# Optimization experiments

Hardware: AMD Instinct MI355X
Metric: run time of the kernel (lower is better)

The kernel has to match this reference:

```python
import jax, jax.numpy as jnp
import numpy as np

# ---- static config (mirrors AdaPKC2D_Thre init) ----
B, IN_CH, OUT_CH = 2, 16, 32
H, W = 256, 256
RB = 1                      # refer_band (must be 1 so ring has N=16 points)
GBH = [1, 2, 3, 4]
GBW = [1, 2, 3, 4]
THRESHOLD = 0.001
INIT_GB = (1, 1)
KH, KW = 4, 4
N = KH * KW                 # 16 sample points per pixel
PAD_H = GBH[-1] + RB        # padding[2]
PAD_W = GBW[-1] + RB        # padding[0]
W_PAD = W + 2 * PAD_W


def _uni_prf_grid(rb, gb):
    """16 (dx,dy) offsets on the guard-band ring (torch _get_uni_prf_grid)."""
    h_prf = (rb + gb[0]) * 2 + 1
    w_prf = (rb + gb[1]) * 2 + 1
    px, py = np.meshgrid(np.arange(-(rb + gb[0]), rb + gb[0] + 1),
                         np.arange(-(rb + gb[1]), rb + gb[1] + 1), indexing='ij')
    idx_td = np.round(np.linspace(0, (rb + gb[1]) * 2, 5)).astype(np.int64)
    idx_lr = np.round(np.linspace(0, (rb + gb[0]) * 2, 5)).astype(np.int64)[1:-1]

    def ring(a):
        return np.concatenate([a[0:rb, idx_td].ravel(),
                               a[idx_lr, w_prf - rb:w_prf].ravel(),
                               a[h_prf - rb:h_prf, idx_td].ravel(),
                               a[idx_lr, 0:rb].ravel()])
    return ring(px), ring(py)


def _build_offsets():
    offs, init_index = [], 0
    for gh in GBH:
        for gw in GBW:
            if gh == INIT_GB[0] and gw == INIT_GB[1]:
                init_index = len(offs)
            dx, dy = _uni_prf_grid(RB, (gh, gw))
            offs.append(dx * W_PAD + dy)  # flattened (row-major) offset
    return np.stack(offs, 0).astype(np.int32), init_index  # (G, N)

OFF_FLAT, INIT_INDEX = _build_offsets()
# flat index of each center pixel in the padded image, (H, W)
CIDX = ((np.arange(H) + PAD_H)[:, None] * W_PAD + (np.arange(W) + PAD_W)[None, :]).astype(np.int32)


def setup_inputs() -> dict:
    key = jax.random.key(0)
    k1, k2, k3 = jax.random.split(key, 3)
    x = jax.random.normal(k1, (B, IN_CH, H, W), dtype=jnp.float32)
    weight = jax.random.normal(k2, (OUT_CH, IN_CH, KH, KW), dtype=jnp.float32) * 0.05
    bias = jax.random.normal(k3, (OUT_CH,), dtype=jnp.float32) * 0.01
    return {"x": x, "weight": weight, "bias": bias}


def reference(x, weight, bias):
    b = x.shape[0]
    x_pad = jnp.pad(x, ((0, 0), (0, 0), (PAD_H, PAD_H), (PAD_W, PAD_W)))
    x_flat = x_pad.reshape(b, IN_CH, -1)                    # (b, c, Hp*Wp)
    cidx = jnp.asarray(CIDX)                                # (H, W)
    off = jnp.asarray(OFF_FLAT)                             # (G, N)

    # center samples (torch x_c has N identical copies; keep one, broadcast)
    x_c = jnp.take_along_axis(x_flat, cidx.reshape(1, 1, -1).astype(jnp.int32),
                              axis=-1).reshape(b, IN_CH, H, W)

    base = cidx[:, :, None]                                 # (H, W, 1)
    sims = []
    for g in range(off.shape[0]):                           # G=16 fixed configs
        idx = (base + off[g][None, None, :]).reshape(1, 1, -1)
        x_r = jnp.take_along_axis(x_flat, idx, axis=-1).reshape(b, IN_CH, H, W, N)
        # sigmoid(mean over channels of x_r * x_c), then mean over the N ring points
        sims.append(jax.nn.sigmoid((x_r * x_c[..., None]).mean(axis=1)).mean(axis=-1))
    sim = jnp.stack(sims, axis=-1)                          # (b, H, W, G)

    order = jnp.argsort(sim, axis=-1)
    sim_sorted = jnp.take_along_axis(sim, order, axis=-1)
    diffs = jnp.diff(sim_sorted, axis=-1)                   # (b, H, W, G-1)
    max_diff = diffs.max(axis=-1)
    max_idx = diffs.argmax(axis=-1)
    ori = jnp.take_along_axis(order, max_idx[..., None], axis=-1)[..., 0]
    ori = jnp.where(max_diff >= THRESHOLD, ori, INIT_INDEX)  # (b, H, W)

    # per-pixel selected guard-band ring -> one gather (torch pr_select pass)
    off_sel = off[ori]                                      # (b, H, W, N)
    idx_sel = (base[None] + off_sel).reshape(b, 1, -1)
    x_rs = jnp.take_along_axis(x_flat, idx_sel, axis=-1).reshape(b, IN_CH, H, W, N)

    x_prf = x_c[..., None] - x_rs                           # (b, c, H, W, N)
    # _reshape_x_prf + 4x4-stride-4 conv == contraction over the N=16 positions
    wk = weight.reshape(OUT_CH, IN_CH, N)
    out = jnp.einsum('bchwn,ocn->bohw', x_prf, wk) + bias[None, :, None, None]
    return out
```

## Files before the change

kernel.cpp:

```cpp
#include <hip/hip_runtime.h>
#include <cstdint>
#include <cstddef>
#include <utility>

#define HH 256
#define WW 256
#define CIN 16
#define COUT 32
#define NB 2
#define TW 32
#define TH 8
#define NPIX (TW*TH)
#define HALO 5
#define LR_ROWS (TH + 2*HALO)
#define LR_COLS (TW + 2*HALO)
#define NCELL (LR_ROWS*LR_COLS)
#define NCELLP 758
#define HW (HH*WW)

typedef float f32x2 __attribute__((ext_vector_type(2)));
typedef float f32x4 __attribute__((ext_vector_type(4)));
typedef float f32x8 __attribute__((ext_vector_type(8)));
typedef int   i32x4 __attribute__((ext_vector_type(4)));
typedef short bf16x8 __attribute__((ext_vector_type(8)));
__device__ __forceinline__ f32x2 splat2(float v) { return f32x2{v, v}; }

__device__ __forceinline__ unsigned short f2bf(float f) {
  unsigned u = __float_as_uint(f);
  return (unsigned short)((u + 0x7fffu + ((u >> 16) & 1u)) >> 16);
}

struct alignas(16) Tables {
  int16_t coff[256];
  int16_t pcoff[128];
  uint8_t gmap[256];
  int np;
};

constexpr int rhe(double v) {
  int f = (int)v;
  double fr = v - (double)f;
  if (fr > 0.5) return f + 1;
  if (fr < 0.5) return f;
  return (f & 1) ? f + 1 : f;
}

constexpr Tables make_tables() {
  Tables t{};
  t.np = 0;
  for (int g = 0; g < 16; ++g) {
    int hp = (g >> 2) + 2;
    int wp = (g & 3) + 2;
    int TD[5] = {}, LRr[3] = {};
    for (int j = 0; j < 5; ++j) TD[j] = rhe(j * wp / 2.0) - wp;
    for (int j = 0; j < 3; ++j) LRr[j] = rhe((j + 1) * hp / 2.0) - hp;
    int dxs[16] = {}, dys[16] = {};
    for (int j = 0; j < 5; ++j) { dxs[j]      = -hp;    dys[j]      = TD[j]; }
    for (int j = 0; j < 3; ++j) { dxs[5 + j]  = LRr[j]; dys[5 + j]  =  wp;   }
    for (int j = 0; j < 5; ++j) { dxs[8 + j]  =  hp;    dys[8 + j]  = TD[j]; }
    for (int j = 0; j < 3; ++j) { dxs[13 + j] = LRr[j]; dys[13 + j] = -wp;   }
    for (int n = 0; n < 16; ++n) {
      int co = dxs[n] * LR_COLS + dys[n];
      t.coff[g * 16 + n] = (int16_t)co;
      int d = -1;
      for (int k = 0; k < t.np; ++k)
        if ((int)t.pcoff[k] == co) { d = k; break; }
      if (d < 0) { d = t.np; t.np++; t.pcoff[d] = (int16_t)co; }
      t.gmap[g * 16 + n] = (uint8_t)d;
    }
  }
  return t;
}

constexpr Tables CT = make_tables();
constexpr int NP = CT.np;
static_assert(NP <= 128, "pair table overflow");
static_assert(NP % 8 == 0, "oct remainder");
__device__ const Tables DT = make_tables();

__device__ __forceinline__ f32x2 numpy_expf2(f32x2 v) {
#pragma clang fp contract(off)
  const f32x2 MAGIC = splat2(12582912.0f);
  f32x2 q = __builtin_elementwise_fma(v, splat2(1.442695040888963407359e+00f), MAGIC);
  q = q - MAGIC;
  f32x2 r = __builtin_elementwise_fma(q, splat2(-6.93145752e-1f), v);
  r = __builtin_elementwise_fma(q, splat2(-1.42860677e-6f), r);
  f32x2 num = __builtin_elementwise_fma(splat2(5.082762527590693718096e-04f), r,
                                        splat2(6.757896990527504603057e-03f));
  num = __builtin_elementwise_fma(num, r, splat2(5.114512081637298353406e-02f));
  num = __builtin_elementwise_fma(num, r, splat2(2.473615434895520810817e-01f));
  num = __builtin_elementwise_fma(num, r, splat2(7.257664613233124478488e-01f));
  num = __builtin_elementwise_fma(num, r, splat2(9.999999999980870924916e-01f));
  f32x2 den = __builtin_elementwise_fma(splat2(2.159509375685829852307e-02f), r,
                                        splat2(-2.742335390411667452936e-01f));
  den = __builtin_elementwise_fma(den, r, splat2(1.0f));
  f32x2 res;
  res.x = ldexpf(num.x / den.x, (int)q.x);
  res.y = ldexpf(num.y / den.y, (int)q.y);
  return res;
}

__device__ __attribute__((noinline))
f32x8 pair8(const float4* __restrict__ xt4,
            int c0, int c1, int c2, int c3, int c4, int c5, int c6, int c7,
            float4 xc0, float4 xc1, float4 xc2, float4 xc3)
{
#pragma clang fp contract(off)
  const f32x2 xcl[8] = { {xc0.x,xc0.y},{xc0.z,xc0.w},{xc1.x,xc1.y},{xc1.z,xc1.w},
                         {xc2.x,xc2.y},{xc2.z,xc2.w},{xc3.x,xc3.y},{xc3.z,xc3.w} };
  const int cells[8] = {c0, c1, c2, c3, c4, c5, c6, c7};
  float mloc[8];
#pragma unroll
  for (int j = 0; j < 8; ++j) {
    const int cell = cells[j];
    float4 R0 = xt4[0 * NCELLP + cell];
    float4 R1 = xt4[1 * NCELLP + cell];
    float4 R2 = xt4[2 * NCELLP + cell];
    float4 R3 = xt4[3 * NCELLP + cell];
    f32x2 pr[8];
    pr[0] = f32x2{R0.x, R0.y} * xcl[0];  pr[1] = f32x2{R0.z, R0.w} * xcl[1];
    pr[2] = f32x2{R1.x, R1.y} * xcl[2];  pr[3] = f32x2{R1.z, R1.w} * xcl[3];
    pr[4] = f32x2{R2.x, R2.y} * xcl[4];  pr[5] = f32x2{R2.z, R2.w} * xcl[5];
    pr[6] = f32x2{R3.x, R3.y} * xcl[6];  pr[7] = f32x2{R3.z, R3.w} * xcl[7];
    float s = pr[0].x;
    s += pr[0].y; s += pr[1].x; s += pr[1].y;
    s += pr[2].x; s += pr[2].y; s += pr[3].x; s += pr[3].y;
    s += pr[4].x; s += pr[4].y; s += pr[5].x; s += pr[5].y;
    s += pr[6].x; s += pr[6].y; s += pr[7].x; s += pr[7].y;
    mloc[j] = s / 16.0f;
  }
  f32x8 outv;
#pragma unroll
  for (int h = 0; h < 4; ++h) {
    f32x2 e = numpy_expf2(-f32x2{mloc[2*h], mloc[2*h+1]});
    f32x2 d = splat2(1.0f) + e;
    outv[2*h]     = 1.0f / d.x;
    outv[2*h + 1] = 1.0f / d.y;
  }
  return outv;
}

template<size_t... BB>
__device__ __forceinline__ void pairs_call(float* sgv, std::index_sequence<BB...>,
    const float4* xt4, int lbase, float4 xc0, float4 xc1, float4 xc2, float4 xc3)
{
  ((void)([&] {
    f32x8 r = pair8(xt4,
                    lbase + (int)CT.pcoff[BB*8 + 0], lbase + (int)CT.pcoff[BB*8 + 1],
                    lbase + (int)CT.pcoff[BB*8 + 2], lbase + (int)CT.pcoff[BB*8 + 3],
                    lbase + (int)CT.pcoff[BB*8 + 4], lbase + (int)CT.pcoff[BB*8 + 5],
                    lbase + (int)CT.pcoff[BB*8 + 6], lbase + (int)CT.pcoff[BB*8 + 7],
                    xc0, xc1, xc2, xc3);
    sgv[BB*8 + 0] = r[0]; sgv[BB*8 + 1] = r[1];
    sgv[BB*8 + 2] = r[2]; sgv[BB*8 + 3] = r[3];
    sgv[BB*8 + 4] = r[4]; sgv[BB*8 + 5] = r[5];
    sgv[BB*8 + 6] = r[6]; sgv[BB*8 + 7] = r[7];
  }()), ...);
}

__global__ void pack_A(const float* __restrict__ w, unsigned short* __restrict__ wsA) {
  int i = blockIdx.x * 256 + threadIdx.x;
  if (i < 2 * 8 * 64 * 8) {
    int m = i >> 12, s = (i >> 9) & 7, l = (i >> 3) & 63, j = i & 7;
    int h = l >> 4, col = l & 15;
    int o = m * 16 + col;
    int n = 2 * s + (h >> 1);
    int c = (h & 1) * 8 + j;
    wsA[i] = f2bf(w[(o * CIN + c) * 16 + n]);
  }
}

__global__ __launch_bounds__(TW * TH)
__attribute__((amdgpu_waves_per_eu(2, 2)))
void adapkc_main(
    const float* __restrict__ x, const unsigned short* __restrict__ wsA,
    const float* __restrict__ bias, float* __restrict__ out)
{
#pragma clang fp contract(off)
  __shared__ float4 xt4[4 * NCELLP];
  __shared__ int    ori_s[NPIX];

  const int tx = threadIdx.x, ty = threadIdx.y;
  const int tid = ty * TW + tx;
  const int b = blockIdx.z;
  const int h0 = blockIdx.y * TH, w0 = blockIdx.x * TW;

  for (int i = tid; i < NCELL; i += TW * TH) {
    int r = i / LR_COLS, cc = i - r * LR_COLS;
    int gh = h0 - HALO + r, gw = w0 - HALO + cc;
    bool ok = (gh >= 0) & (gh < HH) & (gw >= 0) & (gw < WW);
    const float* xp = x + (size_t)b * (CIN * HW) + gh * WW + gw;
#pragma unroll
    for (int q = 0; q < 4; ++q) {
      float4 v = make_float4(0.f, 0.f, 0.f, 0.f);
      if (ok) {
        v.x = xp[(q * 4 + 0) * HW];
        v.y = xp[(q * 4 + 1) * HW];
        v.z = xp[(q * 4 + 2) * HW];
        v.w = xp[(q * 4 + 3) * HW];
      }
      xt4[q * NCELLP + i] = v;
    }
  }
  __syncthreads();

  const int lbase = (ty + HALO) * LR_COLS + (tx + HALO);
  const float4 xc0 = xt4[0 * NCELLP + lbase];
  const float4 xc1 = xt4[1 * NCELLP + lbase];
  const float4 xc2 = xt4[2 * NCELLP + lbase];
  const float4 xc3 = xt4[3 * NCELLP + lbase];

  float sgv[NP];
  pairs_call(sgv, std::make_index_sequence<NP / 8>{}, xt4, lbase, xc0, xc1, xc2, xc3);

  float sim32[16];
#pragma unroll
  for (int g = 0; g < 16; ++g) {
    float A0 = (sgv[CT.gmap[g*16+0]]  + sgv[CT.gmap[g*16+8]])
             + (sgv[CT.gmap[g*16+4]]  + sgv[CT.gmap[g*16+12]]);
    float A1 = (sgv[CT.gmap[g*16+1]]  + sgv[CT.gmap[g*16+9]])
             + (sgv[CT.gmap[g*16+5]]  + sgv[CT.gmap[g*16+13]]);
    float A2 = (sgv[CT.gmap[g*16+2]]  + sgv[CT.gmap[g*16+10]])
             + (sgv[CT.gmap[g*16+6]]  + sgv[CT.gmap[g*16+14]]);
    float A3 = (sgv[CT.gmap[g*16+3]]  + sgv[CT.gmap[g*16+11]])
             + (sgv[CT.gmap[g*16+7]]  + sgv[CT.gmap[g*16+15]]);
    float ssum = (A0 + A2) + (A1 + A3);
    sim32[g] = ssum / 16.0f;
  }

  float s16[16]; int od[16];
#pragma unroll
  for (int i = 0; i < 16; ++i) { s16[i] = sim32[i]; od[i] = i; }
#pragma clang loop unroll(disable)
  for (int p = 0; p < 15; ++p) {
#pragma unroll
    for (int j = 0; j < 15; ++j) {
      float a = s16[j], c = s16[j + 1];
      int oa = od[j], oc = od[j + 1];
      bool sw = a > c;
      s16[j] = sw ? c : a; s16[j + 1] = sw ? a : c;
      od[j] = sw ? oc : oa; od[j + 1] = sw ? oa : oc;
    }
  }
  float best = s16[1] - s16[0]; int ori = od[0];
#pragma unroll
  for (int i = 1; i < 15; ++i) {
    float dd = s16[i + 1] - s16[i];
    if (dd > best) { best = dd; ori = od[i]; }
  }
  if (!(best >= 0.001f)) ori = 0;

  ori_s[tid] = ori;
  __syncthreads();

  const int lane  = tid & 63;
  const int wavei = tid >> 6;
  const int hq  = lane >> 4;
  const int col = lane & 15;
  const int q0  = (hq & 1) * 2;

  bf16x8 afr[2][8];
#pragma unroll
  for (int m = 0; m < 2; ++m)
#pragma unroll
    for (int s = 0; s < 8; ++s)
      afr[m][s] = *(const bf16x8*)(wsA + (((m * 8 + s) * 64 + lane) << 3));

  float bv[2][4];
#pragma unroll
  for (int m = 0; m < 2; ++m)
#pragma unroll
    for (int r = 0; r < 4; ++r) bv[m][r] = bias[m * 16 + hq * 4 + r];

  f32x4 acc[2][4];
#pragma unroll
  for (int m = 0; m < 2; ++m)
#pragma unroll
    for (int t = 0; t < 4; ++t)
      acc[m][t] = f32x4{bv[m][0], bv[m][1], bv[m][2], bv[m][3]};

#pragma unroll
  for (int t = 0; t < 4; ++t) {
    const int p  = wavei * 64 + t * 16 + col;
    const int py = p >> 5, px = p & 31;
    const int lb = (py + HALO) * LR_COLS + (px + HALO);
    const int orip = ori_s[p];
    const int4* cr = (const int4*)&DT.coff[orip * 16];
    int4 cA = cr[0], cB = cr[1];
    int dw[8] = {cA.x, cA.y, cA.z, cA.w, cB.x, cB.y, cB.z, cB.w};
    const float4 xca = xt4[q0 * NCELLP + lb];
    const float4 xcb = xt4[(q0 + 1) * NCELLP + lb];
#pragma unroll
    for (int s = 0; s < 8; ++s) {
      int pk = dw[s];
      int off16 = (hq >= 2) ? (int)(int16_t)((unsigned)pk >> 16)
                            : (int)(int16_t)(pk & 0xffff);
      int cell = lb + off16;
      float4 ra = xt4[q0 * NCELLP + cell];
      float4 rb = xt4[(q0 + 1) * NCELLP + cell];
      f32x2 d0 = f32x2{xca.x, xca.y} - f32x2{ra.x, ra.y};
      f32x2 d1 = f32x2{xca.z, xca.w} - f32x2{ra.z, ra.w};
      f32x2 d2 = f32x2{xcb.x, xcb.y} - f32x2{rb.x, rb.y};
      f32x2 d3 = f32x2{xcb.z, xcb.w} - f32x2{rb.z, rb.w};
      i32x4 wv;
      asm("v_cvt_pk_bf16_f32 %0, %1, %2" : "=v"(wv.x) : "v"(d0.x), "v"(d0.y));
      asm("v_cvt_pk_bf16_f32 %0, %1, %2" : "=v"(wv.y) : "v"(d1.x), "v"(d1.y));
      asm("v_cvt_pk_bf16_f32 %0, %1, %2" : "=v"(wv.z) : "v"(d2.x), "v"(d2.y));
      asm("v_cvt_pk_bf16_f32 %0, %1, %2" : "=v"(wv.w) : "v"(d3.x), "v"(d3.y));
      bf16x8 bfr = __builtin_bit_cast(bf16x8, wv);
      acc[0][t] = __builtin_amdgcn_mfma_f32_16x16x32_bf16(afr[0][s], bfr, acc[0][t], 0, 0, 0);
      acc[1][t] = __builtin_amdgcn_mfma_f32_16x16x32_bf16(afr[1][s], bfr, acc[1][t], 0, 0, 0);
    }
  }

#pragma unroll
  for (int t = 0; t < 4; ++t) {
    const int p  = wavei * 64 + t * 16 + col;
    const int hh = h0 + (p >> 5), ww = w0 + (p & 31);
    float* op = out + (size_t)b * (COUT * HW) + hh * WW + ww;
#pragma unroll
    for (int m = 0; m < 2; ++m)
#pragma unroll
      for (int r = 0; r < 4; ++r)
        op[(m * 16 + hq * 4 + r) * HW] = acc[m][t][r];
  }
}

extern "C" void kernel_launch(void* const* d_in, const int* in_sizes, int n_in,
                              void* d_out, int out_size, void* d_ws, size_t ws_size,
                              hipStream_t stream) {
  const float* x    = (const float*)d_in[0];
  const float* w    = (const float*)d_in[1];
  const float* bias = (const float*)d_in[2];
  float* out = (float*)d_out;
  unsigned short* wsA = (unsigned short*)d_ws;

  hipLaunchKernelGGL(pack_A, dim3(32), dim3(256), 0, stream, w, wsA);

  dim3 grid(WW / TW, HH / TH, NB);
  dim3 block(TW, TH, 1);
  hipLaunchKernelGGL(adapkc_main, grid, block, 0, stream, x, wsA, bias, out);
}
```

Before: 63.21 us.

## Split similarity pairs into two passes with quad-sized helper to cut live registers

Reorders the deduplicated ring-offset table so that offsets needed only by guard-band groups 0-7 come first, then offsets shared with groups 8-15, then offsets used only by groups 8-15. The per-pixel sigmoid similarities are then computed in two passes, with each pass reduced into eight group scores before the next starts. The idea is to shorten the live range of the sgv array and lower register pressure. The noinline helper now handles 4 cells instead of 8 and issues all its LDS loads up front behind a sched_barrier to improve latency hiding. In exchange there are more noinline calls, each with its own call overhead.

```diff
diff --git a/kernel.cpp b/kernel.cpp
--- a/kernel.cpp
+++ b/kernel.cpp
@@ -20,7 +20,6 @@
 
 typedef float f32x2 __attribute__((ext_vector_type(2)));
 typedef float f32x4 __attribute__((ext_vector_type(4)));
-typedef float f32x8 __attribute__((ext_vector_type(8)));
 typedef int   i32x4 __attribute__((ext_vector_type(4)));
 typedef short bf16x8 __attribute__((ext_vector_type(8)));
 __device__ __forceinline__ f32x2 splat2(float v) { return f32x2{v, v}; }
@@ -35,6 +34,7 @@
   int16_t pcoff[128];
   uint8_t gmap[256];
   int np;
+  int npa;
 };
 
 constexpr int rhe(double v) {
@@ -47,7 +47,7 @@
 
 constexpr Tables make_tables() {
   Tables t{};
-  t.np = 0;
+  int coa[256] = {};
   for (int g = 0; g < 16; ++g) {
     int hp = (g >> 2) + 2;
     int wp = (g & 3) + 2;
@@ -61,21 +61,54 @@
     for (int j = 0; j < 3; ++j) { dxs[13 + j] = LRr[j]; dys[13 + j] = -wp;   }
     for (int n = 0; n < 16; ++n) {
       int co = dxs[n] * LR_COLS + dys[n];
+      coa[g * 16 + n] = co;
       t.coff[g * 16 + n] = (int16_t)co;
-      int d = -1;
-      for (int k = 0; k < t.np; ++k)
-        if ((int)t.pcoff[k] == co) { d = k; break; }
-      if (d < 0) { d = t.np; t.np++; t.pcoff[d] = (int16_t)co; }
-      t.gmap[g * 16 + n] = (uint8_t)d;
-    }
-  }
+    }
+  }
+  int16_t A[128] = {}; int na = 0; int amap[128] = {};
+  int16_t B[128] = {}; int nb = 0; int bmap[128] = {};
+  bool ashr[128] = {};
+  int bshA[128] = {};
+  for (int g = 0; g < 8; ++g)
+    for (int n = 0; n < 16; ++n) {
+      int co = coa[g * 16 + n], j = -1;
+      for (int k = 0; k < na; ++k) if ((int)A[k] == co) { j = k; break; }
+      if (j < 0) { j = na++; A[j] = (int16_t)co; }
+      amap[g * 16 + n] = j;
+    }
+  for (int g = 8; g < 16; ++g)
+    for (int n = 0; n < 16; ++n) {
+      int co = coa[g * 16 + n], k = -1;
+      for (int m = 0; m < nb; ++m) if ((int)B[m] == co) { k = m; break; }
+      if (k < 0) { k = nb++; B[k] = (int16_t)co; }
+      bmap[(g - 8) * 16 + n] = k;
+    }
+  for (int k = 0; k < nb; ++k) {
+    bshA[k] = -1;
+    for (int j = 0; j < na; ++j)
+      if (A[j] == B[k]) { bshA[k] = j; ashr[j] = true; break; }
+  }
+  int posA[128] = {}, posB[128] = {};
+  int p = 0;
+  for (int j = 0; j < na; ++j) if (!ashr[j]) posA[j] = p++;
+  for (int j = 0; j < na; ++j) if (ashr[j])  posA[j] = p++;
+  t.npa = p;
+  for (int k = 0; k < nb; ++k) posB[k] = (bshA[k] >= 0) ? posA[bshA[k]] : p++;
+  t.np = p;
+  for (int j = 0; j < na; ++j) t.pcoff[posA[j]] = A[j];
+  for (int k = 0; k < nb; ++k) t.pcoff[posB[k]] = B[k];
+  for (int g = 0; g < 8; ++g)
+    for (int n = 0; n < 16; ++n) t.gmap[g * 16 + n] = (uint8_t)posA[amap[g * 16 + n]];
+  for (int g = 8; g < 16; ++g)
+    for (int n = 0; n < 16; ++n) t.gmap[g * 16 + n] = (uint8_t)posB[bmap[(g - 8) * 16 + n]];
   return t;
 }
 
 constexpr Tables CT = make_tables();
-constexpr int NP = CT.np;
-static_assert(NP <= 128, "pair table overflow");
-static_assert(NP % 8 == 0, "oct remainder");
+constexpr int NP  = CT.np;
+constexpr int NPA = CT.npa;
+static_assert(NP <= 128 && NP % 4 == 0, "pair table");
+static_assert(NPA % 4 == 0, "pass-1 boundary not quad-aligned");
 __device__ const Tables DT = make_tables();
 
 __device__ __forceinline__ f32x2 numpy_expf2(f32x2 v) {
@@ -101,22 +134,29 @@
 }
 
 __device__ __attribute__((noinline))
-f32x8 pair8(const float4* __restrict__ xt4,
-            int c0, int c1, int c2, int c3, int c4, int c5, int c6, int c7,
-            float4 xc0, float4 xc1, float4 xc2, float4 xc3)
+float4 pair4(const float4* __restrict__ xt4, int c0, int c1, int c2, int c3,
+             float4 xc0, float4 xc1, float4 xc2, float4 xc3)
 {
 #pragma clang fp contract(off)
+  float4 Ra0 = xt4[0 * NCELLP + c0], Ra1 = xt4[1 * NCELLP + c0];
+  float4 Ra2 = xt4[2 * NCELLP + c0], Ra3 = xt4[3 * NCELLP + c0];
+  float4 Rb0 = xt4[0 * NCELLP + c1], Rb1 = xt4[1 * NCELLP + c1];
+  float4 Rb2 = xt4[2 * NCELLP + c1], Rb3 = xt4[3 * NCELLP + c1];
+  float4 Rc0 = xt4[0 * NCELLP + c2], Rc1 = xt4[1 * NCELLP + c2];
+  float4 Rc2 = xt4[2 * NCELLP + c2], Rc3 = xt4[3 * NCELLP + c2];
+  float4 Rd0 = xt4[0 * NCELLP + c3], Rd1 = xt4[1 * NCELLP + c3];
+  float4 Rd2 = xt4[2 * NCELLP + c3], Rd3 = xt4[3 * NCELLP + c3];
+  __builtin_amdgcn_sched_barrier(0);
+
   const f32x2 xcl[8] = { {xc0.x,xc0.y},{xc0.z,xc0.w},{xc1.x,xc1.y},{xc1.z,xc1.w},
                          {xc2.x,xc2.y},{xc2.z,xc2.w},{xc3.x,xc3.y},{xc3.z,xc3.w} };
-  const int cells[8] = {c0, c1, c2, c3, c4, c5, c6, c7};
-  float mloc[8];
-#pragma unroll
-  for (int j = 0; j < 8; ++j) {
-    const int cell = cells[j];
-    float4 R0 = xt4[0 * NCELLP + cell];
-    float4 R1 = xt4[1 * NCELLP + cell];
-    float4 R2 = xt4[2 * NCELLP + cell];
-    float4 R3 = xt4[3 * NCELLP + cell];
+  float mloc[4];
+#pragma unroll
+  for (int j = 0; j < 4; ++j) {
+    float4 R0 = (j == 0) ? Ra0 : (j == 1) ? Rb0 : (j == 2) ? Rc0 : Rd0;
+    float4 R1 = (j == 0) ? Ra1 : (j == 1) ? Rb1 : (j == 2) ? Rc1 : Rd1;
+    float4 R2 = (j == 0) ? Ra2 : (j == 1) ? Rb2 : (j == 2) ? Rc2 : Rd2;
+    float4 R3 = (j == 0) ? Ra3 : (j == 1) ? Rb3 : (j == 2) ? Rc3 : Rd3;
     f32x2 pr[8];
     pr[0] = f32x2{R0.x, R0.y} * xcl[0];  pr[1] = f32x2{R0.z, R0.w} * xcl[1];
     pr[2] = f32x2{R1.x, R1.y} * xcl[2];  pr[3] = f32x2{R1.z, R1.w} * xcl[3];
@@ -129,93 +169,37 @@
     s += pr[6].x; s += pr[6].y; s += pr[7].x; s += pr[7].y;
     mloc[j] = s / 16.0f;
   }
-  f32x8 outv;
-#pragma unroll
-  for (int h = 0; h < 4; ++h) {
-    f32x2 e = numpy_expf2(-f32x2{mloc[2*h], mloc[2*h+1]});
-    f32x2 d = splat2(1.0f) + e;
-    outv[2*h]     = 1.0f / d.x;
-    outv[2*h + 1] = 1.0f / d.y;
-  }
+  f32x2 e0 = numpy_expf2(-f32x2{mloc[0], mloc[1]});
+  f32x2 e1 = numpy_expf2(-f32x2{mloc[2], mloc[3]});
+  f32x2 d0 = splat2(1.0f) + e0;
+  f32x2 d1 = splat2(1.0f) + e1;
+  float4 outv;
+  outv.x = 1.0f / d0.x; outv.y = 1.0f / d0.y;
+  outv.z = 1.0f / d1.x; outv.w = 1.0f / d1.y;
   return outv;
 }
 
-template<size_t... BB>
+template<int OFS, size_t... BB>
 __device__ __forceinline__ void pairs_call(float* sgv, std::index_sequence<BB...>,
     const float4* xt4, int lbase, float4 xc0, float4 xc1, float4 xc2, float4 xc3)
 {
   ((void)([&] {
-    f32x8 r = pair8(xt4,
-                    lbase + (int)CT.pcoff[BB*8 + 0], lbase + (int)CT.pcoff[BB*8 + 1],
-                    lbase + (int)CT.pcoff[BB*8 + 2], lbase + (int)CT.pcoff[BB*8 + 3],
-                    lbase + (int)CT.pcoff[BB*8 + 4], lbase + (int)CT.pcoff[BB*8 + 5],
-                    lbase + (int)CT.pcoff[BB*8 + 6], lbase + (int)CT.pcoff[BB*8 + 7],
-                    xc0, xc1, xc2, xc3);
-    sgv[BB*8 + 0] = r[0]; sgv[BB*8 + 1] = r[1];
-    sgv[BB*8 + 2] = r[2]; sgv[BB*8 + 3] = r[3];
-    sgv[BB*8 + 4] = r[4]; sgv[BB*8 + 5] = r[5];
-    sgv[BB*8 + 6] = r[6]; sgv[BB*8 + 7] = r[7];
+    float4 r = pair4(xt4,
+                     lbase + (int)CT.pcoff[OFS + BB*4 + 0], lbase + (int)CT.pcoff[OFS + BB*4 + 1],
+                     lbase + (int)CT.pcoff[OFS + BB*4 + 2], lbase + (int)CT.pcoff[OFS + BB*4 + 3],
+                     xc0, xc1, xc2, xc3);
+    sgv[OFS + BB*4 + 0] = r.x; sgv[OFS + BB*4 + 1] = r.y;
+    sgv[OFS + BB*4 + 2] = r.z; sgv[OFS + BB*4 + 3] = r.w;
   }()), ...);
 }
 
-__global__ void pack_A(const float* __restrict__ w, unsigned short* __restrict__ wsA) {
-  int i = blockIdx.x * 256 + threadIdx.x;
-  if (i < 2 * 8 * 64 * 8) {
-    int m = i >> 12, s = (i >> 9) & 7, l = (i >> 3) & 63, j = i & 7;
-    int h = l >> 4, col = l & 15;
-    int o = m * 16 + col;
-    int n = 2 * s + (h >> 1);
-    int c = (h & 1) * 8 + j;
-    wsA[i] = f2bf(w[(o * CIN + c) * 16 + n]);
-  }
-}
-
-__global__ __launch_bounds__(TW * TH)
-__attribute__((amdgpu_waves_per_eu(2, 2)))
-void adapkc_main(
-    const float* __restrict__ x, const unsigned short* __restrict__ wsA,
-    const float* __restrict__ bias, float* __restrict__ out)
+template<int G0>
+__device__ __forceinline__ void reduce8(float* sim32, const float* sgv)
 {
 #pragma clang fp contract(off)
-  __shared__ float4 xt4[4 * NCELLP];
-  __shared__ int    ori_s[NPIX];
-
-  const int tx = threadIdx.x, ty = threadIdx.y;
-  const int tid = ty * TW + tx;
-  const int b = blockIdx.z;
-  const int h0 = blockIdx.y * TH, w0 = blockIdx.x * TW;
-
-  for (int i = tid; i < NCELL; i += TW * TH) {
-    int r = i / LR_COLS, cc = i - r * LR_COLS;
-    int gh = h0 - HALO + r, gw = w0 - HALO + cc;
-    bool ok = (gh >= 0) & (gh < HH) & (gw >= 0) & (gw < WW);
-    const float* xp = x + (size_t)b * (CIN * HW) + gh * WW + gw;
-#pragma unroll
-    for (int q = 0; q < 4; ++q) {
-      float4 v = make_float4(0.f, 0.f, 0.f, 0.f);
-      if (ok) {
-        v.x = xp[(q * 4 + 0) * HW];
-        v.y = xp[(q * 4 + 1) * HW];
-        v.z = xp[(q * 4 + 2) * HW];
-        v.w = xp[(q * 4 + 3) * HW];
-      }
-      xt4[q * NCELLP + i] = v;
-    }
-  }
-  __syncthreads();
-
-  const int lbase = (ty + HALO) * LR_COLS + (tx + HALO);
-  const float4 xc0 = xt4[0 * NCELLP + lbase];
-  const float4 xc1 = xt4[1 * NCELLP + lbase];
-  const float4 xc2 = xt4[2 * NCELLP + lbase];
-  const float4 xc3 = xt4[3 * NCELLP + lbase];
-
-  float sgv[NP];
-  pairs_call(sgv, std::make_index_sequence<NP / 8>{}, xt4, lbase, xc0, xc1, xc2, xc3);
-
-  float sim32[16];
-#pragma unroll
-  for (int g = 0; g < 16; ++g) {
+#pragma unroll
+  for (int gg = 0; gg < 8; ++gg) {
+    const int g = G0 + gg;
     float A0 = (sgv[CT.gmap[g*16+0]]  + sgv[CT.gmap[g*16+8]])
              + (sgv[CT.gmap[g*16+4]]  + sgv[CT.gmap[g*16+12]]);
     float A1 = (sgv[CT.gmap[g*16+1]]  + sgv[CT.gmap[g*16+9]])
@@ -227,6 +211,68 @@
     float ssum = (A0 + A2) + (A1 + A3);
     sim32[g] = ssum / 16.0f;
   }
+}
+
+__global__ void pack_A(const float* __restrict__ w, unsigned short* __restrict__ wsA) {
+  int i = blockIdx.x * 256 + threadIdx.x;
+  if (i < 2 * 8 * 64 * 8) {
+    int m = i >> 12, s = (i >> 9) & 7, l = (i >> 3) & 63, j = i & 7;
+    int h = l >> 4, col = l & 15;
+    int o = m * 16 + col;
+    int n = 2 * s + (h >> 1);
+    int c = (h & 1) * 8 + j;
+    wsA[i] = f2bf(w[(o * CIN + c) * 16 + n]);
+  }
+}
+
+__global__ __launch_bounds__(TW * TH)
+__attribute__((amdgpu_waves_per_eu(2, 2)))
+void adapkc_main(
+    const float* __restrict__ x, const unsigned short* __restrict__ wsA,
+    const float* __restrict__ bias, float* __restrict__ out)
+{
+#pragma clang fp contract(off)
+  __shared__ float4 xt4[4 * NCELLP];
+  __shared__ int    ori_s[NPIX];
+
+  const int tx = threadIdx.x, ty = threadIdx.y;
+  const int tid = ty * TW + tx;
+  const int b = blockIdx.z;
+  const int h0 = blockIdx.y * TH, w0 = blockIdx.x * TW;
+
+  for (int i = tid; i < NCELL; i += TW * TH) {
+    int r = i / LR_COLS, cc = i - r * LR_COLS;
+    int gh = h0 - HALO + r, gw = w0 - HALO + cc;
+    bool ok = (gh >= 0) & (gh < HH) & (gw >= 0) & (gw < WW);
+    const float* xp = x + (size_t)b * (CIN * HW) + gh * WW + gw;
+#pragma unroll
+    for (int q = 0; q < 4; ++q) {
+      float4 v = make_float4(0.f, 0.f, 0.f, 0.f);
+      if (ok) {
+        v.x = xp[(q * 4 + 0) * HW];
+        v.y = xp[(q * 4 + 1) * HW];
+        v.z = xp[(q * 4 + 2) * HW];
+        v.w = xp[(q * 4 + 3) * HW];
+      }
+      xt4[q * NCELLP + i] = v;
+    }
+  }
+  __syncthreads();
+
+  const int lbase = (ty + HALO) * LR_COLS + (tx + HALO);
+  const float4 xc0 = xt4[0 * NCELLP + lbase];
+  const float4 xc1 = xt4[1 * NCELLP + lbase];
+  const float4 xc2 = xt4[2 * NCELLP + lbase];
+  const float4 xc3 = xt4[3 * NCELLP + lbase];
+
+  float sgv[NP];
+  float sim32[16];
+  pairs_call<0>(sgv, std::make_index_sequence<NPA / 4>{},
+                xt4, lbase, xc0, xc1, xc2, xc3);
+  reduce8<0>(sim32, sgv);
+  pairs_call<NPA>(sgv, std::make_index_sequence<(NP - NPA) / 4>{},
+                  xt4, lbase, xc0, xc1, xc2, xc3);
+  reduce8<8>(sim32, sgv);
 
   float s16[16]; int od[16];
 #pragma unroll
```

Result: faster. 60.39 us (-4.5%).
